# Optimization experiments

Measured on AMD Instinct MI355X. Metric: run time of the kernel, lower is better.

## Reference

```python
import jax, jax.numpy as jnp
import numpy as np
import math

B, S, DM, H, N_HASHES, BUCKET = 1, 1024, 512, 8, 8, 64
HD = DM // H
N_BUCKETS = max(2, 2 * (S // (2 * BUCKET)))   # 16
ROT = max(1, N_BUCKETS // 2)                  # 8


def setup_inputs() -> dict:
    key = jax.random.key(0)
    ks = jax.random.split(key, 6)
    sc = 1.0 / math.sqrt(DM)
    return {
        "x": jax.random.normal(ks[0], (B, S, DM), dtype=jnp.float32),
        "w_qk": (jax.random.normal(ks[1], (DM, DM), dtype=jnp.float32) * sc),
        "b_qk": jnp.zeros((DM,), dtype=jnp.float32),
        "w_v": (jax.random.normal(ks[2], (DM, DM), dtype=jnp.float32) * sc),
        "b_v": jnp.zeros((DM,), dtype=jnp.float32),
        "w_o": (jax.random.normal(ks[3], (DM, DM), dtype=jnp.float32) * sc),
        "b_o": jnp.zeros((DM,), dtype=jnp.float32),
        # random rotations used for LSH hashing (torch.randn in hash_vectors)
        "rotations": jax.random.normal(ks[4], (N_HASHES, H, HD, ROT), dtype=jnp.float32),
    }


def reference(x, w_qk, b_qk, w_v, b_v, w_o, b_o, rotations):
    # projections, split heads: (B, H, S, HD)
    qk = (x @ w_qk + b_qk).reshape(B, S, H, HD).transpose(0, 2, 1, 3)
    v = (x @ w_v + b_v).reshape(B, S, H, HD).transpose(0, 2, 1, 3)

    # LSH bucket assignment: (B, H, S, n_hashes)
    rot = jnp.einsum('bhnd,rhdc->bhnrc', qk, rotations)
    rot = jnp.concatenate([rot, -rot], axis=-1)
    buckets = jnp.argmax(rot, axis=-1)

    # The original gathers (batch, head, pos) jointly per bucket, so attention
    # mixes across batch and head; flatten exactly the same way.
    N = B * H * S
    qkf = qk.reshape(N, HD)
    vf = v.reshape(N, HD)
    bkf = buckets.reshape(N, N_HASHES).T  # (n_hashes, N)

    # dots are shared across hash rounds; only the bucket mask changes
    dots = (qkf @ qkf.T) / math.sqrt(HD)  # (N, N)

    def body(acc, bk):
        same = bk[:, None] == bk[None, :]  # bucket-equality mask
        w = jax.nn.softmax(jnp.where(same, dots, -jnp.inf), axis=-1)
        return acc + w @ vf, None

    out, _ = jax.lax.scan(body, jnp.zeros_like(vf), bkf)
    out = out / N_HASHES

    out = out.reshape(B, H, S, HD).transpose(0, 2, 1, 3).reshape(B, S, DM)
    return out @ w_o + b_o
```

## Files before the change

kernel.cpp:

```cpp
#include <hip/hip_runtime.h>
#include <math.h>

#define S 1024
#define DM 512
#define H 8
#define HD 64
#define NH 8
#define NB 16
#define N 8192
#define SCALE 0.125f
#define EXP2C 0.18033688f

typedef __attribute__((ext_vector_type(4))) float f32x4;
typedef __attribute__((ext_vector_type(8))) short s16x8;
typedef __attribute__((ext_vector_type(4))) short s16x4;

__device__ __forceinline__ short f2bf(float f) {
  union { float f; unsigned u; } a; a.f = f;
  unsigned r = a.u + 0x7fffu + ((a.u >> 16) & 1u);
  return (short)(r >> 16);
}
__device__ __forceinline__ float bf2f(short h) {
  union { unsigned u; float f; } a; a.u = ((unsigned)(unsigned short)h) << 16;
  return a.f;
}
__device__ __forceinline__ int f2bf2(float lo, float hi) {
  return (int)(unsigned short)f2bf(lo) | (((int)f2bf(hi)) << 16);
}
__device__ __forceinline__ short lev_bf(float v, int lev) {
  short h0 = f2bf(v);
  if (lev == 0) return h0;
  float r1 = v - bf2f(h0);
  short h1 = f2bf(r1);
  if (lev == 1) return h1;
  return f2bf(r1 - bf2f(h1));
}

#if __has_builtin(__builtin_amdgcn_mfma_f32_16x16x16_bf16)
#define MFMA_PV(a, b, c) __builtin_amdgcn_mfma_f32_16x16x16_bf16(a, b, c, 0, 0, 0)
#else
#define MFMA_PV(a, b, c) __builtin_amdgcn_mfma_f32_16x16x16bf16_1k(a, b, c, 0, 0, 0)
#endif

__global__ __launch_bounds__(256) void wprep_kernel(
    const float* __restrict__ wqk, const float* __restrict__ wv,
    const float* __restrict__ wo,
    short* __restrict__ wtqk, short* __restrict__ wtv, short* __restrict__ wto,
    int* __restrict__ cz) {
  int tid = threadIdx.x;
  if (blockIdx.x == 0) cz[tid] = 0;
  int mat = blockIdx.x >> 6;
  int tile = blockIdx.x & 63;
  int kt = tile >> 3, dt = tile & 7;
  const float* w = (mat == 0) ? wqk : ((mat == 1) ? wv : wo);

  __shared__ float wlds[64 * 68];
  int kr = tid >> 2, c4 = tid & 3;
  const float4* src = (const float4*)(w + (size_t)(kt * 64 + kr) * DM + dt * 64 + c4 * 16);
#pragma unroll
  for (int i = 0; i < 4; ++i) {
    float4 v = src[i];
    float* d = &wlds[kr * 68 + c4 * 16 + i * 4];
    d[0] = v.x; d[1] = v.y; d[2] = v.z; d[3] = v.w;
  }
  __syncthreads();
  int dr = tid >> 2, kc = tid & 3;
  s16x8 h0a, h0b, h1a, h1b, h2a, h2b;
#pragma unroll
  for (int i = 0; i < 8; ++i) {
    float v = wlds[(kc * 16 + i) * 68 + dr];
    short a = f2bf(v); float r1 = v - bf2f(a);
    short b = f2bf(r1); short c = f2bf(r1 - bf2f(b));
    h0a[i] = a; h1a[i] = b; h2a[i] = c;
  }
#pragma unroll
  for (int i = 0; i < 8; ++i) {
    float v = wlds[(kc * 16 + 8 + i) * 68 + dr];
    short a = f2bf(v); float r1 = v - bf2f(a);
    short b = f2bf(r1); short c = f2bf(r1 - bf2f(b));
    h0b[i] = a; h1b[i] = b; h2b[i] = c;
  }
  size_t dst = (size_t)(dt * 64 + dr) * DM + kt * 64 + kc * 16;
  if (mat == 0) {
    s16x8* p0 = (s16x8*)(wtqk + dst);
    s16x8* p1 = (s16x8*)(wtqk + (size_t)DM * DM + dst);
    s16x8* p2 = (s16x8*)(wtqk + (size_t)2 * DM * DM + dst);
    p0[0] = h0a; p0[1] = h0b; p1[0] = h1a; p1[1] = h1b; p2[0] = h2a; p2[1] = h2b;
  } else if (mat == 1) {
    s16x8* p = (s16x8*)(wtv + dst); p[0] = h0a; p[1] = h0b;
  } else {
    s16x8* p = (s16x8*)(wto + dst); p[0] = h0a; p[1] = h0b;
  }
}

#define PST 72
__global__ __launch_bounds__(256) void projmm_kernel(
    const float* __restrict__ x, const short* __restrict__ wtqk,
    const short* __restrict__ wtv,
    const float* __restrict__ bqk, const float* __restrict__ bv,
    float* __restrict__ qkpart, short* __restrict__ vb) {
  int mt = blockIdx.x & 15;
  int rest = blockIdx.x >> 4;
  int sp = rest >> 3;
  int head = rest & 7;
  bool isv = (sp == 6);
  int xl = isv ? 0 : ((0x210100 >> (sp << 2)) & 0xF);
  int wl = isv ? 0 : ((0x012010 >> (sp << 2)) & 0xF);
  const short* wt = isv ? wtv : (wtqk + (size_t)wl * DM * DM);

  __shared__ short a_lds[2][64 * PST];
  __shared__ short b_lds[2][64 * PST];

  int tid = threadIdx.x;
  int wave = tid >> 6, lane = tid & 63;
  int col = lane & 15, quad = lane >> 4;
  int mh = wave & 1, nh2 = wave >> 1;

  f32x4 acc[2][2];
#pragma unroll
  for (int i = 0; i < 2; ++i)
#pragma unroll
    for (int j = 0; j < 2; ++j) acc[i][j] = (f32x4){0.f, 0.f, 0.f, 0.f};

  int sr = tid >> 2, c4 = tid & 3;
  int gran = sr * PST + ((c4 ^ (sr & 3)) << 4);

  {
    const float4* xp = (const float4*)(x + (size_t)(mt * 64 + sr) * DM + c4 * 16);
    float4 f0 = xp[0], f1 = xp[1], f2 = xp[2], f3 = xp[3];
    float vv[16] = {f0.x,f0.y,f0.z,f0.w, f1.x,f1.y,f1.z,f1.w,
                    f2.x,f2.y,f2.z,f2.w, f3.x,f3.y,f3.z,f3.w};
    s16x8 ha, hb;
#pragma unroll
    for (int i = 0; i < 8; ++i) { ha[i] = lev_bf(vv[i], xl); hb[i] = lev_bf(vv[8 + i], xl); }
    s16x8* ad = (s16x8*)&a_lds[0][gran];
    ad[0] = ha; ad[1] = hb;
    const s16x8* wp = (const s16x8*)(wt + (size_t)(head * 64 + sr) * DM + c4 * 16);
    s16x8* bd = (s16x8*)&b_lds[0][gran];
    bd[0] = wp[0]; bd[1] = wp[1];
  }
  __syncthreads();

  for (int ci = 0; ci < 8; ++ci) {
    int cur = ci & 1, nxt = cur ^ 1;
    float4 pf0, pf1, pf2, pf3; s16x8 pw0, pw1;
    bool has = (ci + 1) < 8;
    if (has) {
      int kc = ci + 1;
      const float4* xp = (const float4*)(x + (size_t)(mt * 64 + sr) * DM + kc * 64 + c4 * 16);
      pf0 = xp[0]; pf1 = xp[1]; pf2 = xp[2]; pf3 = xp[3];
      const s16x8* wp = (const s16x8*)(wt + (size_t)(head * 64 + sr) * DM + kc * 64 + c4 * 16);
      pw0 = wp[0]; pw1 = wp[1];
    }
#pragma unroll
    for (int s2 = 0; s2 < 2; ++s2) {
      s16x8 af[2], bfv[2];
#pragma unroll
      for (int mi = 0; mi < 2; ++mi) {
        int row = mh * 32 + mi * 16 + col;
        int cidx = ((s2 << 1) + (quad >> 1)) ^ (row & 3);
        af[mi] = *(const s16x8*)&a_lds[cur][row * PST + (cidx << 4) + ((quad & 1) << 3)];
      }
#pragma unroll
      for (int ni = 0; ni < 2; ++ni) {
        int row = nh2 * 32 + ni * 16 + col;
        int cidx = ((s2 << 1) + (quad >> 1)) ^ (row & 3);
        bfv[ni] = *(const s16x8*)&b_lds[cur][row * PST + (cidx << 4) + ((quad & 1) << 3)];
      }
#pragma unroll
      for (int mi = 0; mi < 2; ++mi)
#pragma unroll
        for (int ni = 0; ni < 2; ++ni)
          acc[mi][ni] = __builtin_amdgcn_mfma_f32_16x16x32_bf16(af[mi], bfv[ni],
                                                               acc[mi][ni], 0, 0, 0);
    }
    if (has) {
      float vv[16] = {pf0.x,pf0.y,pf0.z,pf0.w, pf1.x,pf1.y,pf1.z,pf1.w,
                      pf2.x,pf2.y,pf2.z,pf2.w, pf3.x,pf3.y,pf3.z,pf3.w};
      s16x8 ha, hb;
#pragma unroll
      for (int i = 0; i < 8; ++i) { ha[i] = lev_bf(vv[i], xl); hb[i] = lev_bf(vv[8 + i], xl); }
      s16x8* ad = (s16x8*)&a_lds[nxt][gran];
      ad[0] = ha; ad[1] = hb;
      s16x8* bd = (s16x8*)&b_lds[nxt][gran];
      bd[0] = pw0; bd[1] = pw1;
    }
    __syncthreads();
  }
  if (isv) {
#pragma unroll
    for (int ni = 0; ni < 2; ++ni) {
      int nl = nh2 * 32 + ni * 16 + col;
      float bb = bv[head * 64 + nl];
#pragma unroll
      for (int mi = 0; mi < 2; ++mi)
#pragma unroll
        for (int u = 0; u < 4; ++u) {
          int s = mt * 64 + mh * 32 + mi * 16 + quad * 4 + u;
          vb[((size_t)head * S + s) * HD + nl] = f2bf(acc[mi][ni][u] + bb);
        }
    }
  } else {
    float* dst = qkpart + (size_t)sp * N * HD;
#pragma unroll
    for (int ni = 0; ni < 2; ++ni) {
      int nl = nh2 * 32 + ni * 16 + col;
      float bb = (sp == 0) ? bqk[head * 64 + nl] : 0.f;
#pragma unroll
      for (int mi = 0; mi < 2; ++mi)
#pragma unroll
        for (int u = 0; u < 4; ++u) {
          int s = mt * 64 + mh * 32 + mi * 16 + quad * 4 + u;
          dst[((size_t)head * S + s) * HD + nl] = acc[mi][ni][u] + bb;
        }
    }
  }
}

__global__ __launch_bounds__(256) void sumslab_kernel(
    const float* __restrict__ qkpart, float* __restrict__ qkf,
    short* __restrict__ qkb) {
  int idx = blockIdx.x * 256 + threadIdx.x;
  f32x4 s = ((const f32x4*)qkpart)[idx];
#pragma unroll
  for (int sl = 1; sl < 6; ++sl)
    s += ((const f32x4*)(qkpart + (size_t)sl * N * HD))[idx];
  ((f32x4*)qkf)[idx] = s;
  int2 pk = make_int2(f2bf2(s[0], s[1]), f2bf2(s[2], s[3]));
  *(int2*)(qkb + (size_t)idx * 4) = pk;
}

__global__ __launch_bounds__(256) void bucket_kernel(
    const float* __restrict__ qkf, const float* __restrict__ rot,
    int* __restrict__ cursor, int* __restrict__ perm2) {
  __shared__ float Rl[HD * 8];
  __shared__ int lcnt[NB];
  __shared__ int gbase[NB];
  int tid = threadIdx.x;
  int g = blockIdx.x * 256 + tid;
  int n = g & (N - 1);
  int r = g >> 13;
  int h = n >> 10;
  const float* R = rot + (size_t)((r * H + h) * HD) * 8;
  if (tid < 128) ((f32x4*)Rl)[tid] = ((const f32x4*)R)[tid];
  if (tid < NB) lcnt[tid] = 0;

  f32x4 qv[16];
  const f32x4* q4 = (const f32x4*)(qkf + (size_t)n * HD);
#pragma unroll
  for (int d4 = 0; d4 < 16; ++d4) qv[d4] = q4[d4];
  __syncthreads();

  float v[8];
#pragma unroll
  for (int c = 0; c < 8; ++c) v[c] = 0.f;
#pragma unroll
  for (int d4 = 0; d4 < 16; ++d4) {
    f32x4 q = qv[d4];
#pragma unroll
    for (int j = 0; j < 4; ++j) {
      const f32x4* Rr = (const f32x4*)&Rl[(d4 * 4 + j) * 8];
      f32x4 r0 = Rr[0], r1 = Rr[1];
      float qj = q[j];
#pragma unroll
      for (int c = 0; c < 4; ++c) v[c] = fmaf(qj, r0[c], v[c]);
#pragma unroll
      for (int c = 0; c < 4; ++c) v[4 + c] = fmaf(qj, r1[c], v[4 + c]);
    }
  }
  float best = v[0];
  int bi = 0;
#pragma unroll
  for (int c = 1; c < 16; ++c) {
    float val = (c < 8) ? v[c] : -v[c - 8];
    if (val > best) { best = val; bi = c; }
  }

  int lrank = atomicAdd(&lcnt[bi], 1);
  __syncthreads();
  if (tid < NB) gbase[tid] = atomicAdd(&cursor[(r << 4) + tid], lcnt[tid]);
  __syncthreads();
  perm2[(((size_t)(r << 4) + bi) << 13) + gbase[bi] + lrank] = n;
}

#define KT 64
#define KST 72
#define VTS2 72
#define VBUF (64 * VTS2)
__global__ __launch_bounds__(512) void attn_kernel(
    const short* __restrict__ qkb, const short* __restrict__ vb,
    const int* __restrict__ perm2, const int* __restrict__ cursor,
    short* __restrict__ accumB) {
  int bx = blockIdx.x;
  int rb = bx & 127;
  int chunk = bx >> 7;
  int r = rb >> 4;
  int b = rb & 15;
  int cnt = cursor[rb];
  int q0 = chunk << 7;
  if (q0 >= cnt) return;
  const int* plist = perm2 + ((size_t)rb << 13);

  int tid = threadIdx.x;
  int wave = tid >> 6, lane = tid & 63;
  int col = lane & 15, quad = lane >> 4;

  __shared__ short k_lds[2][KT * KST];
  __shared__ short v_lds[2][VBUF];

  int qslot = q0 + (wave << 4) + col;
  bool qvalid = qslot < cnt;
  int qidx = plist[qvalid ? qslot : 0];
  bool wactive = (q0 + (wave << 4)) < cnt;

  for (int e = tid; e < VBUF; e += 512) ((int*)v_lds)[e] = 0;

  s16x8 qa[2];
#pragma unroll
  for (int s2 = 0; s2 < 2; ++s2)
    qa[s2] = *(const s16x8*)(qkb + (size_t)qidx * HD + s2 * 32 + quad * 8);
  __syncthreads();

  float lsum = 0.f;
  f32x4 o0 = {0,0,0,0}, o1 = {0,0,0,0}, o2 = {0,0,0,0}, o3 = {0,0,0,0};

  int jsk = tid >> 2, csk = tid & 3;
  bool stager = tid < 256;
  int kgran = jsk * KST + ((csk ^ (jsk & 3)) << 4);
  int ksw0 = (jsk + 24 * csk) & 63;
  int ksw1 = (jsk + 24 * csk + 4) & 63;
  int vdr = csk * 16 * VTS2;

  int vrow = col * VTS2;
  int vco = (col >> 3) << 2;

  {
    int nj = min(KT, cnt);
    if (stager && jsk < nj) {
      int gk = plist[jsk];
      const s16x8* kp = (const s16x8*)(qkb + (size_t)gk * HD + (csk << 4));
      const s16x8* vp = (const s16x8*)(vb + (size_t)gk * HD + (csk << 4));
      s16x8 a0 = kp[0], a1 = kp[1], b0 = vp[0], b1 = vp[1];
      s16x8* kd = (s16x8*)&k_lds[0][kgran];
      kd[0] = a0; kd[1] = a1;
      short* vt = &v_lds[0][vdr];
#pragma unroll
      for (int i = 0; i < 8; ++i) {
        vt[i * VTS2 + ksw0] = b0[i];
        vt[(8 + i) * VTS2 + ksw1] = b1[i];
      }
    }
  }
  __syncthreads();

  int ntiles = (cnt + KT - 1) >> 6;
  for (int t = 0; t < ntiles; ++t) {
    int jt = t << 6;
    int cur = t & 1, nxt = cur ^ 1;
    s16x8 a0, a1, b0, b1;
    bool pf_ok = false;
    int jn = jt + KT;
    if (jn < cnt && stager) {
      int njn = min(KT, cnt - jn);
      if (jsk < njn) {
        pf_ok = true;
        int gk = plist[jn + jsk];
        const s16x8* kp = (const s16x8*)(qkb + (size_t)gk * HD + (csk << 4));
        const s16x8* vp = (const s16x8*)(vb + (size_t)gk * HD + (csk << 4));
        a0 = kp[0]; a1 = kp[1]; b0 = vp[0]; b1 = vp[1];
      }
    }
    if (wactive) {
      const short* vtc = v_lds[cur];
      int c_hi = min(4, (cnt - jt + 15) >> 4);
      for (int c16 = 0; c16 < c_hi; ++c16) {
        int k0s = (c16 << 4) + (quad << 2) + vco;
        s16x4 vf0 = *(const s16x4*)&vtc[vrow + ((k0s) & 63)];
        s16x4 vf1 = *(const s16x4*)&vtc[1 * 16 * VTS2 + vrow + ((k0s + 24) & 63)];
        s16x4 vf2 = *(const s16x4*)&vtc[2 * 16 * VTS2 + vrow + ((k0s + 48) & 63)];
        s16x4 vf3 = *(const s16x4*)&vtc[3 * 16 * VTS2 + vrow + ((k0s + 72) & 63)];

        f32x4 sacc = {0,0,0,0};
        int key = (c16 << 4) + col;
        const short* kb = &k_lds[cur][key * KST];
#pragma unroll
        for (int s2 = 0; s2 < 2; ++s2) {
          int cidx = ((s2 << 1) + (quad >> 1)) ^ (key & 3);
          s16x8 kf = *(const s16x8*)&kb[(cidx << 4) + ((quad & 1) << 3)];
          sacc = __builtin_amdgcn_mfma_f32_16x16x32_bf16(kf, qa[s2], sacc, 0, 0, 0);
        }
        int kbase = jt + (c16 << 4) + (quad << 2);
        float pw[4];
        if (kbase + 4 <= cnt) {
#pragma unroll
          for (int u = 0; u < 4; ++u) pw[u] = exp2f(sacc[u] * EXP2C);
        } else {
#pragma unroll
          for (int u = 0; u < 4; ++u)
            pw[u] = (kbase + u < cnt) ? exp2f(sacc[u] * EXP2C) : 0.f;
        }
        lsum += (pw[0] + pw[1]) + (pw[2] + pw[3]);
        s16x4 pfr;
        pfr[0] = f2bf(pw[0]); pfr[1] = f2bf(pw[1]);
        pfr[2] = f2bf(pw[2]); pfr[3] = f2bf(pw[3]);
        o0 = MFMA_PV(pfr, vf0, o0);
        o1 = MFMA_PV(pfr, vf1, o1);
        o2 = MFMA_PV(pfr, vf2, o2);
        o3 = MFMA_PV(pfr, vf3, o3);
      }
    }
    if (pf_ok) {
      s16x8* kd = (s16x8*)&k_lds[nxt][kgran];
      kd[0] = a0; kd[1] = a1;
      short* vt = &v_lds[nxt][vdr];
#pragma unroll
      for (int i = 0; i < 8; ++i) {
        vt[i * VTS2 + ksw0] = b0[i];
        vt[(8 + i) * VTS2 + ksw1] = b1[i];
      }
    }
    __syncthreads();
  }

  lsum += __shfl_xor(lsum, 16);
  lsum += __shfl_xor(lsum, 32);
  float inv = 1.f / lsum;
#pragma unroll
  for (int u = 0; u < 4; ++u) {
    int slot = (quad << 2) + u;
    int spos = q0 + (wave << 4) + slot;
    float inv_u = __shfl(inv, slot);
    int qidx_u = __shfl(qidx, slot);
    if (spos < cnt) {
      short* dst = accumB + ((size_t)r * N + qidx_u) * HD + col;
      dst[0]  = f2bf(o0[u] * inv_u);
      dst[16] = f2bf(o1[u] * inv_u);
      dst[32] = f2bf(o2[u] * inv_u);
      dst[48] = f2bf(o3[u] * inv_u);
    }
  }
}

__global__ __launch_bounds__(256) void outproj_kernel(
    const short* __restrict__ accumB, const short* __restrict__ wto,
    const float* __restrict__ bo, float* __restrict__ out) {
  int mt = blockIdx.x & 31;
  int nt = blockIdx.x >> 5;
  __shared__ short a_lds[2][32 * PST];
  __shared__ short b_lds[2][64 * PST];
  int tid = threadIdx.x;
  int wave = tid >> 6, lane = tid & 63;
  int col = lane & 15, quad = lane >> 4;
  int mi2 = wave & 1, nh2 = wave >> 1;

  f32x4 acc[2];
  acc[0] = (f32x4){0.f,0.f,0.f,0.f};
  acc[1] = (f32x4){0.f,0.f,0.f,0.f};

  bool isA = tid < 128;
  int sr = tid >> 2, c4 = tid & 3;
  int agran = sr * PST + ((c4 ^ (sr & 3)) << 4);
  int dl = (tid - 128) >> 1, gp = tid & 1;

  {
    if (isA) {
      size_t abase = ((size_t)0 * S + mt * 32 + sr) * HD + c4 * 16;
      float a16[16];
#pragma unroll
      for (int i = 0; i < 16; ++i) a16[i] = 0.f;
#pragma unroll
      for (int r = 0; r < NH; ++r) {
        const short* ap = accumB + (size_t)r * N * HD + abase;
        s16x8 h0 = *(const s16x8*)ap, h1 = *(const s16x8*)(ap + 8);
#pragma unroll
        for (int i = 0; i < 8; ++i) { a16[i] += bf2f(h0[i]); a16[8 + i] += bf2f(h1[i]); }
      }
      s16x8 ha, hb;
#pragma unroll
      for (int i = 0; i < 8; ++i) {
        ha[i] = f2bf(a16[i] * 0.125f); hb[i] = f2bf(a16[8 + i] * 0.125f);
      }
      s16x8* ad = (s16x8*)&a_lds[0][agran];
      ad[0] = ha; ad[1] = hb;
    } else {
      const s16x8* wp = (const s16x8*)(wto + (size_t)(nt * 64 + dl) * DM + gp * 32);
      int g0 = gp * 2;
      s16x8* d0 = (s16x8*)&b_lds[0][dl * PST + ((g0 ^ (dl & 3)) << 4)];
      d0[0] = wp[0]; d0[1] = wp[1];
      s16x8* d1 = (s16x8*)&b_lds[0][dl * PST + (((g0 + 1) ^ (dl & 3)) << 4)];
      d1[0] = wp[2]; d1[1] = wp[3];
    }
  }
  __syncthreads();

  for (int kc = 0; kc < 8; ++kc) {
    int cur = kc & 1, nxt = cur ^ 1;
    bool has = kc + 1 < 8;
    float a16[16];
    s16x8 pb0, pb1, pb2, pb3;
    if (has) {
      if (isA) {
        size_t abase = ((size_t)(kc + 1) * S + mt * 32 + sr) * HD + c4 * 16;
#pragma unroll
        for (int i = 0; i < 16; ++i) a16[i] = 0.f;
#pragma unroll
        for (int r = 0; r < NH; ++r) {
          const short* ap = accumB + (size_t)r * N * HD + abase;
          s16x8 h0 = *(const s16x8*)ap, h1 = *(const s16x8*)(ap + 8);
#pragma unroll
          for (int i = 0; i < 8; ++i) { a16[i] += bf2f(h0[i]); a16[8 + i] += bf2f(h1[i]); }
        }
      } else {
        const s16x8* wp = (const s16x8*)(wto + (size_t)(nt * 64 + dl) * DM +
                                         (kc + 1) * 64 + gp * 32);
        pb0 = wp[0]; pb1 = wp[1]; pb2 = wp[2]; pb3 = wp[3];
      }
    }
#pragma unroll
    for (int s2 = 0; s2 < 2; ++s2) {
      int arow = mi2 * 16 + col;
      int acidx = ((s2 << 1) + (quad >> 1)) ^ (arow & 3);
      s16x8 af = *(const s16x8*)&a_lds[cur][arow * PST + (acidx << 4) + ((quad & 1) << 3)];
      s16x8 bfv[2];
#pragma unroll
      for (int ni = 0; ni < 2; ++ni) {
        int brow = nh2 * 32 + ni * 16 + col;
        int bcidx = ((s2 << 1) + (quad >> 1)) ^ (brow & 3);
        bfv[ni] = *(const s16x8*)&b_lds[cur][brow * PST + (bcidx << 4) + ((quad & 1) << 3)];
      }
#pragma unroll
      for (int ni = 0; ni < 2; ++ni)
        acc[ni] = __builtin_amdgcn_mfma_f32_16x16x32_bf16(af, bfv[ni], acc[ni], 0, 0, 0);
    }
    if (has) {
      if (isA) {
        s16x8 ha, hb;
#pragma unroll
        for (int i = 0; i < 8; ++i) {
          ha[i] = f2bf(a16[i] * 0.125f); hb[i] = f2bf(a16[8 + i] * 0.125f);
        }
        s16x8* ad = (s16x8*)&a_lds[nxt][agran];
        ad[0] = ha; ad[1] = hb;
      } else {
        int g0 = gp * 2;
        s16x8* d0 = (s16x8*)&b_lds[nxt][dl * PST + ((g0 ^ (dl & 3)) << 4)];
        d0[0] = pb0; d0[1] = pb1;
        s16x8* d1 = (s16x8*)&b_lds[nxt][dl * PST + (((g0 + 1) ^ (dl & 3)) << 4)];
        d1[0] = pb2; d1[1] = pb3;
      }
    }
    __syncthreads();
  }
#pragma unroll
  for (int ni = 0; ni < 2; ++ni) {
    int nl = nh2 * 32 + ni * 16 + col;
    int dgl = nt * 64 + nl;
    float bb = bo[dgl];
#pragma unroll
    for (int u = 0; u < 4; ++u) {
      int s = mt * 32 + mi2 * 16 + quad * 4 + u;
      out[(size_t)s * DM + dgl] = acc[ni][u] + bb;
    }
  }
}

extern "C" void kernel_launch(void* const* d_in, const int* in_sizes, int n_in,
                              void* d_out, int out_size, void* d_ws, size_t ws_size,
                              hipStream_t stream) {
  const float* x    = (const float*)d_in[0];
  const float* w_qk = (const float*)d_in[1];
  const float* b_qk = (const float*)d_in[2];
  const float* w_v  = (const float*)d_in[3];
  const float* b_v  = (const float*)d_in[4];
  const float* w_o  = (const float*)d_in[5];
  const float* b_o  = (const float*)d_in[6];
  const float* rot  = (const float*)d_in[7];
  float* out = (float*)d_out;

  char* ws = (char*)d_ws;
  const size_t MB = 1024u * 1024u;
  short* qkb    = (short*)(ws);
  short* vb     = (short*)(ws + 1 * MB);
  float* qkpart = (float*)(ws + 2 * MB);
  short* accumB = (short*)(ws + 2 * MB);
  int* perm2    = (int*)(ws + 10 * MB);
  float* qkf    = (float*)(ws + 18 * MB);
  short* wtqk   = (short*)(ws + 20 * MB);
  short* wtv    = (short*)(ws + 20 * MB + 1536u * 1024);
  short* wto    = (short*)(ws + 22 * MB);
  int* cursor   = (int*)(ws + 22 * MB + 512u * 1024);

  wprep_kernel<<<192, 256, 0, stream>>>(w_qk, w_v, w_o, wtqk, wtv, wto, cursor);
  projmm_kernel<<<896, 256, 0, stream>>>(x, wtqk, wtv, b_qk, b_v, qkpart, vb);
  sumslab_kernel<<<512, 256, 0, stream>>>(qkpart, qkf, qkb);
  bucket_kernel<<<(NH * N) / 256, 256, 0, stream>>>(qkf, rot, cursor, perm2);
  attn_kernel<<<64 * 128, 512, 0, stream>>>(qkb, vb, perm2, cursor, accumB);
  outproj_kernel<<<256, 256, 0, stream>>>(accumB, wto, b_o, out);
}
```

Measured before the change: 146.9 us.

## Prefetch permutation indices a tile ahead and batch QK/softmax/PV stages per tile

```diff
diff --git a/kernel.cpp b/kernel.cpp
--- a/kernel.cpp
+++ b/kernel.cpp
@@ -295,7 +295,6 @@
   int rb = bx & 127;
   int chunk = bx >> 7;
   int r = rb >> 4;
-  int b = rb & 15;
   int cnt = cursor[rb];
   int q0 = chunk << 7;
   if (q0 >= cnt) return;
@@ -327,8 +326,8 @@
   int jsk = tid >> 2, csk = tid & 3;
   bool stager = tid < 256;
   int kgran = jsk * KST + ((csk ^ (jsk & 3)) << 4);
-  int ksw0 = (jsk + 24 * csk) & 63;
-  int ksw1 = (jsk + 24 * csk + 4) & 63;
+  int ksw0 = (jsk + 16 * csk) & 63;
+  int ksw1 = (jsk + 16 * csk + 4) & 63;
   int vdr = csk * 16 * VTS2;
 
   int vrow = col * VTS2;
@@ -351,6 +350,12 @@
       }
     }
   }
+  int pln = 0; bool pln_ok = false;
+  if (stager) {
+    int i1 = KT + jsk;
+    pln_ok = i1 < cnt;
+    pln = plist[i1 < 8192 ? i1 : 8191];
+  }
   __syncthreads();
 
   int ntiles = (cnt + KT - 1) >> 6;
@@ -358,56 +363,55 @@
     int jt = t << 6;
     int cur = t & 1, nxt = cur ^ 1;
     s16x8 a0, a1, b0, b1;
-    bool pf_ok = false;
-    int jn = jt + KT;
-    if (jn < cnt && stager) {
-      int njn = min(KT, cnt - jn);
-      if (jsk < njn) {
-        pf_ok = true;
-        int gk = plist[jn + jsk];
-        const s16x8* kp = (const s16x8*)(qkb + (size_t)gk * HD + (csk << 4));
-        const s16x8* vp = (const s16x8*)(vb + (size_t)gk * HD + (csk << 4));
-        a0 = kp[0]; a1 = kp[1]; b0 = vp[0]; b1 = vp[1];
-      }
+    bool pf_ok = stager && pln_ok;
+    if (pf_ok) {
+      const s16x8* kp = (const s16x8*)(qkb + (size_t)pln * HD + (csk << 4));
+      const s16x8* vp = (const s16x8*)(vb + (size_t)pln * HD + (csk << 4));
+      a0 = kp[0]; a1 = kp[1]; b0 = vp[0]; b1 = vp[1];
+    }
+    int pl2 = 0; bool pl2_ok = false;
+    if (stager) {
+      int i2 = jt + 2 * KT + jsk;
+      pl2_ok = i2 < cnt;
+      pl2 = plist[i2 < 8192 ? i2 : 8191];
     }
     if (wactive) {
       const short* vtc = v_lds[cur];
-      int c_hi = min(4, (cnt - jt + 15) >> 4);
-      for (int c16 = 0; c16 < c_hi; ++c16) {
-        int k0s = (c16 << 4) + (quad << 2) + vco;
-        s16x4 vf0 = *(const s16x4*)&vtc[vrow + ((k0s) & 63)];
-        s16x4 vf1 = *(const s16x4*)&vtc[1 * 16 * VTS2 + vrow + ((k0s + 24) & 63)];
-        s16x4 vf2 = *(const s16x4*)&vtc[2 * 16 * VTS2 + vrow + ((k0s + 48) & 63)];
-        s16x4 vf3 = *(const s16x4*)&vtc[3 * 16 * VTS2 + vrow + ((k0s + 72) & 63)];
-
-        f32x4 sacc = {0,0,0,0};
-        int key = (c16 << 4) + col;
-        const short* kb = &k_lds[cur][key * KST];
-#pragma unroll
-        for (int s2 = 0; s2 < 2; ++s2) {
-          int cidx = ((s2 << 1) + (quad >> 1)) ^ (key & 3);
-          s16x8 kf = *(const s16x8*)&kb[(cidx << 4) + ((quad & 1) << 3)];
-          sacc = __builtin_amdgcn_mfma_f32_16x16x32_bf16(kf, qa[s2], sacc, 0, 0, 0);
-        }
-        int kbase = jt + (c16 << 4) + (quad << 2);
-        float pw[4];
-        if (kbase + 4 <= cnt) {
-#pragma unroll
-          for (int u = 0; u < 4; ++u) pw[u] = exp2f(sacc[u] * EXP2C);
-        } else {
-#pragma unroll
-          for (int u = 0; u < 4; ++u)
-            pw[u] = (kbase + u < cnt) ? exp2f(sacc[u] * EXP2C) : 0.f;
-        }
-        lsum += (pw[0] + pw[1]) + (pw[2] + pw[3]);
-        s16x4 pfr;
-        pfr[0] = f2bf(pw[0]); pfr[1] = f2bf(pw[1]);
-        pfr[2] = f2bf(pw[2]); pfr[3] = f2bf(pw[3]);
-        o0 = MFMA_PV(pfr, vf0, o0);
-        o1 = MFMA_PV(pfr, vf1, o1);
-        o2 = MFMA_PV(pfr, vf2, o2);
-        o3 = MFMA_PV(pfr, vf3, o3);
-      }
+      const short* ktc = k_lds[cur];
+      f32x4 sA = {0,0,0,0}, sB = {0,0,0,0}, sC = {0,0,0,0}, sD = {0,0,0,0};
+#define QK1(C, SA) { int key = ((C) << 4) + col; \
+      const short* kb = &ktc[key * KST]; \
+      { int cidx = (quad >> 1) ^ (key & 3); \
+        s16x8 kf = *(const s16x8*)&kb[(cidx << 4) + ((quad & 1) << 3)]; \
+        SA = __builtin_amdgcn_mfma_f32_16x16x32_bf16(kf, qa[0], SA, 0, 0, 0); } \
+      { int cidx = (2 + (quad >> 1)) ^ (key & 3); \
+        s16x8 kf = *(const s16x8*)&kb[(cidx << 4) + ((quad & 1) << 3)]; \
+        SA = __builtin_amdgcn_mfma_f32_16x16x32_bf16(kf, qa[1], SA, 0, 0, 0); } }
+      QK1(0, sA) QK1(1, sB) QK1(2, sC) QK1(3, sD)
+      s16x4 p0, p1, p2, p3;
+#define SM1(C, SA, PF) { int kbase = jt + ((C) << 4) + (quad << 2); \
+      float pw[4]; \
+      if (kbase + 4 <= cnt) { \
+        _Pragma("unroll") for (int u = 0; u < 4; ++u) pw[u] = exp2f(SA[u] * EXP2C); \
+      } else { \
+        _Pragma("unroll") for (int u = 0; u < 4; ++u) \
+          pw[u] = (kbase + u < cnt) ? exp2f(SA[u] * EXP2C) : 0.f; \
+      } \
+      lsum += (pw[0] + pw[1]) + (pw[2] + pw[3]); \
+      PF[0] = f2bf(pw[0]); PF[1] = f2bf(pw[1]); \
+      PF[2] = f2bf(pw[2]); PF[3] = f2bf(pw[3]); }
+      SM1(0, sA, p0) SM1(1, sB, p1) SM1(2, sC, p2) SM1(3, sD, p3)
+#define PV1(C, PF) { int k0s = ((C) << 4) + (quad << 2) + vco; \
+      s16x4 va = *(const s16x4*)&vtc[vrow + (k0s & 63)]; \
+      s16x4 vb_ = *(const s16x4*)&vtc[16 * VTS2 + vrow + ((k0s + 16) & 63)]; \
+      s16x4 vc = *(const s16x4*)&vtc[32 * VTS2 + vrow + ((k0s + 32) & 63)]; \
+      s16x4 vd = *(const s16x4*)&vtc[48 * VTS2 + vrow + ((k0s + 48) & 63)]; \
+      o0 = MFMA_PV(PF, va, o0); o1 = MFMA_PV(PF, vb_, o1); \
+      o2 = MFMA_PV(PF, vc, o2); o3 = MFMA_PV(PF, vd, o3); }
+      PV1(0, p0) PV1(1, p1) PV1(2, p2) PV1(3, p3)
+#undef QK1
+#undef SM1
+#undef PV1
     }
     if (pf_ok) {
       s16x8* kd = (s16x8*)&k_lds[nxt][kgran];
@@ -419,6 +423,7 @@
         vt[(8 + i) * VTS2 + ksw1] = b1[i];
       }
     }
+    pln = pl2; pln_ok = pl2_ok;
     __syncthreads();
   }
 
```

New measurement: 144.2 us. No clear change (-1.9%).
